# Kernel optimization log

Measured on AMD Instinct MI355X. Metric: run time of the kernel, lower is better.

The kernel has to match this reference:

```python
import jax, jax.numpy as jnp
import numpy as np


def setup_inputs() -> dict:
    key = jax.random.key(0)
    k1, k2 = jax.random.split(key)
    B, S, V = 8, 512, 30522
    logits = jax.random.normal(k1, (B, S, V), dtype=jnp.float32)
    attention_mask = jax.random.randint(k2, (B, S), 0, 2, dtype=jnp.int32)
    return {"logits": logits, "attention_mask": attention_mask, "top_k": 64}


def reference(logits, attention_mask, top_k):
    # Fused SPLADE activation: log1p(relu(logits)) * mask, max-pooled over seq.
    mask = attention_mask.astype(logits.dtype)[:, :, None]        # (B, S, 1)
    activated = jnp.log1p(jax.nn.relu(logits)) * mask             # (B, S, V)
    values = jnp.max(activated, axis=1)                           # (B, V)
    # Top-k thresholding: zero out everything below the k-th largest value.
    top_values, _ = jax.lax.top_k(values, top_k)                  # (B, k)
    threshold = top_values[..., -1, None]                         # (B, 1)
    return values * (values >= threshold).astype(values.dtype)
```

## Files before the change

kernel.cpp:

```cpp
#include <hip/hip_runtime.h>
#include <hip/hip_bf16.h>

constexpr int B_  = 8;
constexpr int S_  = 512;
constexpr int V_  = 30522;
constexpr int V2_ = V_ / 2;
constexpr int V4_ = V_ / 4;

typedef float f32x4 __attribute__((ext_vector_type(4)));

constexpr int K1_THREADS = 1024;
constexpr int VSPLIT  = 4;
constexpr int SLICE4  = 1908;
constexpr int NSCHUNK = 8;
constexpr int SCHUNK  = S_ / NSCHUNK;
constexpr int NSLOT   = 2;

__global__ __launch_bounds__(K1_THREADS)
void splade_max_atomic(const float* __restrict__ logits,
                       const int* __restrict__ mask,
                       unsigned int* __restrict__ out_bits)
{
    __shared__ int s_idx[SCHUNK];
    __shared__ int s_cnt;
    const int vs = blockIdx.x;
    const int sc = blockIdx.y;
    const int b  = blockIdx.z;
    const int s0 = sc * SCHUNK;

    if (threadIdx.x < 64) {
        const int lane = threadIdx.x;
        const int m = mask[b * S_ + s0 + lane] != 0;
        const unsigned long long bal = __ballot(m);
        if (m) s_idx[(int)__popcll(bal & ((1ull << lane) - 1ull))] = lane;
        if (lane == 0) s_cnt = (int)__popcll(bal);
    }
    __syncthreads();
    const int n = s_cnt;

    const int len4 = (vs == VSPLIT - 1) ? (V4_ - vs * SLICE4) : SLICE4;
    int  col4[NSLOT];
    bool valid[NSLOT];
#pragma unroll
    for (int p = 0; p < NSLOT; ++p) {
        const int idx4 = threadIdx.x + p * K1_THREADS;
        valid[p] = (idx4 < len4);
        col4[p]  = valid[p] ? (vs * SLICE4 + idx4) : 0;
    }

    f32x4 acc[NSLOT];
#pragma unroll
    for (int p = 0; p < NSLOT; ++p) acc[p] = (f32x4)(0.f);

    const bool do_tail = (vs == VSPLIT - 1) && (threadIdx.x == 0);
    float tail0 = 0.f, tail1 = 0.f;

    int r = 0;
    for (; r + 1 < n; r += 2) {
        const int s0i = s_idx[r], s1i = s_idx[r + 1];
        const float* r0 = logits + (size_t)(b * S_ + s0 + s0i) * V_;
        const float* r1 = logits + (size_t)(b * S_ + s0 + s1i) * V_;
        f32x4 x0[NSLOT], x1[NSLOT];
#pragma unroll
        for (int p = 0; p < NSLOT; ++p)
            x0[p] = *reinterpret_cast<const f32x4*>(r0 + 4 * col4[p]);
#pragma unroll
        for (int p = 0; p < NSLOT; ++p)
            x1[p] = *reinterpret_cast<const f32x4*>(r1 + 4 * col4[p]);
        if (do_tail) {
            const float2 t0 = *reinterpret_cast<const float2*>(r0 + 2 * (V2_ - 1));
            const float2 t1 = *reinterpret_cast<const float2*>(r1 + 2 * (V2_ - 1));
            tail0 = fmaxf(tail0, fmaxf(t0.x, t1.x));
            tail1 = fmaxf(tail1, fmaxf(t0.y, t1.y));
        }
#pragma unroll
        for (int p = 0; p < NSLOT; ++p) {
#pragma unroll
            for (int q = 0; q < 4; ++q)
                acc[p][q] = fmaxf(acc[p][q], fmaxf(x0[p][q], x1[p][q]));
        }
    }
    if (r < n) {
        const float* r0 = logits + (size_t)(b * S_ + s0 + s_idx[r]) * V_;
        f32x4 x0[NSLOT];
#pragma unroll
        for (int p = 0; p < NSLOT; ++p)
            x0[p] = *reinterpret_cast<const f32x4*>(r0 + 4 * col4[p]);
        if (do_tail) {
            const float2 t0 = *reinterpret_cast<const float2*>(r0 + 2 * (V2_ - 1));
            tail0 = fmaxf(tail0, t0.x);
            tail1 = fmaxf(tail1, t0.y);
        }
#pragma unroll
        for (int p = 0; p < NSLOT; ++p) {
#pragma unroll
            for (int q = 0; q < 4; ++q)
                acc[p][q] = fmaxf(acc[p][q], x0[p][q]);
        }
    }

    unsigned int* o = out_bits + (size_t)b * V_;
#pragma unroll
    for (int p = 0; p < NSLOT; ++p) {
        if (valid[p]) {
#pragma unroll
            for (int q = 0; q < 4; ++q)
                atomicMax(o + 4 * col4[p] + q, __float_as_uint(acc[p][q]));
        }
    }
    if (do_tail) {
        atomicMax(o + 2 * (V2_ - 1),     __float_as_uint(tail0));
        atomicMax(o + 2 * (V2_ - 1) + 1, __float_as_uint(tail1));
    }
}

constexpr int K2_BLOCK = 1024;
constexpr int NPT2 = (V2_ + K2_BLOCK - 1) / K2_BLOCK;

__global__ __launch_bounds__(K2_BLOCK)
void splade_topk_kernel(unsigned int* __restrict__ out_bits,
                        const int* __restrict__ topk_ptr)
{
    const int b = blockIdx.x;
    const int k = topk_ptr[0];
    uint2* row2 = reinterpret_cast<uint2*>(out_bits) + (size_t)b * V2_;

    unsigned int v[2 * NPT2];
#pragma unroll
    for (int i = 0; i < NPT2; ++i) {
        const int idx2 = threadIdx.x + i * K2_BLOCK;
        uint2 x = make_uint2(0u, 0u);
        if (idx2 < V2_) x = row2[idx2];
        v[2 * i]     = x.x;
        v[2 * i + 1] = x.y;
    }

    __shared__ int s_cnt[32];
    for (int i = threadIdx.x; i < 32; i += K2_BLOCK) s_cnt[i] = 0;
    __syncthreads();

    unsigned int lo = 0u, hi = 0x7f800000u;
    for (int it = 0; it < 32; ++it) {
        if (hi - lo <= 1u) break;
        const unsigned int mid = lo + ((hi - lo) >> 1);
        int c = 0;
#pragma unroll
        for (int i = 0; i < 2 * NPT2; ++i)
            c += (int)__popcll(__ballot(v[i] >= mid));
        if ((threadIdx.x & 63) == 0) atomicAdd(&s_cnt[it], c);
        __syncthreads();
        const int cnt = s_cnt[it];
        if (cnt >= k) lo = mid; else hi = mid;
    }

    const unsigned int T = lo;
    float2* frow2 = reinterpret_cast<float2*>(row2);
#pragma unroll
    for (int i = 0; i < NPT2; ++i) {
        const int idx2 = threadIdx.x + i * K2_BLOCK;
        if (idx2 < V2_) {
            const unsigned int a = v[2 * i], c = v[2 * i + 1];
            float rx = 0.0f, ry = 0.0f;
            if (a >= T) rx = log1pf(__uint_as_float(a));
            if (c >= T) ry = log1pf(__uint_as_float(c));
            frow2[idx2] = make_float2(rx, ry);
        }
    }
}

extern "C" void kernel_launch(void* const* d_in, const int* in_sizes, int n_in,
                              void* d_out, int out_size, void* d_ws, size_t ws_size,
                              hipStream_t stream) {
    const float* logits = (const float*)d_in[0];
    const int*   mask   = (const int*)d_in[1];
    const int*   topk   = (const int*)d_in[2];
    unsigned int* out   = (unsigned int*)d_out;

    hipMemsetAsync(out, 0, (size_t)out_size * sizeof(float), stream);

    dim3 g1(VSPLIT, NSCHUNK, B_);
    splade_max_atomic<<<g1, K1_THREADS, 0, stream>>>(logits, mask, out);
    splade_topk_kernel<<<B_, K2_BLOCK, 0, stream>>>(out, topk);
}
```

Baseline: 93.01 us.

## Replace atomicMax reduction with per-chunk partial buffers plus a merge kernel

The seq-max kernel now writes per-sequence-chunk partial maxima into workspace with vector stores instead of issuing scalar atomicMax into the output, and doubles the number of sequence chunks for more blocks. A new merge kernel reduces the 16 partials per (batch, vocab) element, which also removes the memset. This trades atomic traffic for an extra kernel launch and roughly 16x B x V of partial writes and reads.

```diff
diff --git a/kernel.cpp b/kernel.cpp
--- a/kernel.cpp
+++ b/kernel.cpp
@@ -12,14 +12,14 @@
 constexpr int K1_THREADS = 1024;
 constexpr int VSPLIT  = 4;
 constexpr int SLICE4  = 1908;
-constexpr int NSCHUNK = 8;
+constexpr int NSCHUNK = 16;
 constexpr int SCHUNK  = S_ / NSCHUNK;
 constexpr int NSLOT   = 2;
 
 __global__ __launch_bounds__(K1_THREADS)
-void splade_max_atomic(const float* __restrict__ logits,
-                       const int* __restrict__ mask,
-                       unsigned int* __restrict__ out_bits)
+void splade_partial_max(const float* __restrict__ logits,
+                        const int* __restrict__ mask,
+                        float* __restrict__ partial)
 {
     __shared__ int s_idx[SCHUNK];
     __shared__ int s_cnt;
@@ -30,7 +30,7 @@
 
     if (threadIdx.x < 64) {
         const int lane = threadIdx.x;
-        const int m = mask[b * S_ + s0 + lane] != 0;
+        const int m = (lane < SCHUNK) ? (mask[b * S_ + s0 + lane] != 0) : 0;
         const unsigned long long bal = __ballot(m);
         if (m) s_idx[(int)__popcll(bal & ((1ull << lane) - 1ull))] = lane;
         if (lane == 0) s_cnt = (int)__popcll(bal);
@@ -99,40 +99,56 @@
         }
     }
 
-    unsigned int* o = out_bits + (size_t)b * V_;
-#pragma unroll
-    for (int p = 0; p < NSLOT; ++p) {
-        if (valid[p]) {
-#pragma unroll
-            for (int q = 0; q < 4; ++q)
-                atomicMax(o + 4 * col4[p] + q, __float_as_uint(acc[p][q]));
-        }
-    }
+    float* dst = partial + ((size_t)sc * B_ + b) * V_;
+#pragma unroll
+    for (int p = 0; p < NSLOT; ++p)
+        if (valid[p])
+            *reinterpret_cast<f32x4*>(dst + 4 * col4[p]) = acc[p];
     if (do_tail) {
-        atomicMax(o + 2 * (V2_ - 1),     __float_as_uint(tail0));
-        atomicMax(o + 2 * (V2_ - 1) + 1, __float_as_uint(tail1));
-    }
+        dst[2 * (V2_ - 1)]     = tail0;
+        dst[2 * (V2_ - 1) + 1] = tail1;
+    }
+}
+
+constexpr int KM_THREADS  = 256;
+constexpr int KM_BLOCKS_X = (V2_ + KM_THREADS - 1) / KM_THREADS;
+
+__global__ __launch_bounds__(KM_THREADS)
+void splade_merge(const float* __restrict__ partial, float* __restrict__ out)
+{
+    const int b    = blockIdx.y;
+    const int idx2 = blockIdx.x * KM_THREADS + threadIdx.x;
+    if (idx2 >= V2_) return;
+    const float2* p0 = reinterpret_cast<const float2*>(partial) + (size_t)b * V2_ + idx2;
+    float2 m = make_float2(0.0f, 0.0f);
+#pragma unroll
+    for (int gg = 0; gg < NSCHUNK; ++gg) {
+        const float2 x = p0[(size_t)gg * B_ * V2_];
+        m.x = fmaxf(m.x, x.x);
+        m.y = fmaxf(m.y, x.y);
+    }
+    reinterpret_cast<float2*>(out)[(size_t)b * V2_ + idx2] = m;
 }
 
 constexpr int K2_BLOCK = 1024;
 constexpr int NPT2 = (V2_ + K2_BLOCK - 1) / K2_BLOCK;
 
 __global__ __launch_bounds__(K2_BLOCK)
-void splade_topk_kernel(unsigned int* __restrict__ out_bits,
+void splade_topk_kernel(float* __restrict__ out,
                         const int* __restrict__ topk_ptr)
 {
     const int b = blockIdx.x;
     const int k = topk_ptr[0];
-    uint2* row2 = reinterpret_cast<uint2*>(out_bits) + (size_t)b * V2_;
+    float2* row2 = reinterpret_cast<float2*>(out) + (size_t)b * V2_;
 
     unsigned int v[2 * NPT2];
 #pragma unroll
     for (int i = 0; i < NPT2; ++i) {
         const int idx2 = threadIdx.x + i * K2_BLOCK;
-        uint2 x = make_uint2(0u, 0u);
+        float2 x = make_float2(0.0f, 0.0f);
         if (idx2 < V2_) x = row2[idx2];
-        v[2 * i]     = x.x;
-        v[2 * i + 1] = x.y;
+        v[2 * i]     = __float_as_uint(x.x);
+        v[2 * i + 1] = __float_as_uint(x.y);
     }
 
     __shared__ int s_cnt[32];
@@ -154,7 +170,6 @@
     }
 
     const unsigned int T = lo;
-    float2* frow2 = reinterpret_cast<float2*>(row2);
 #pragma unroll
     for (int i = 0; i < NPT2; ++i) {
         const int idx2 = threadIdx.x + i * K2_BLOCK;
@@ -163,7 +178,7 @@
             float rx = 0.0f, ry = 0.0f;
             if (a >= T) rx = log1pf(__uint_as_float(a));
             if (c >= T) ry = log1pf(__uint_as_float(c));
-            frow2[idx2] = make_float2(rx, ry);
+            row2[idx2] = make_float2(rx, ry);
         }
     }
 }
@@ -174,11 +189,12 @@
     const float* logits = (const float*)d_in[0];
     const int*   mask   = (const int*)d_in[1];
     const int*   topk   = (const int*)d_in[2];
-    unsigned int* out   = (unsigned int*)d_out;
-
-    hipMemsetAsync(out, 0, (size_t)out_size * sizeof(float), stream);
+    float*       out    = (float*)d_out;
+    float*       ws     = (float*)d_ws;
 
     dim3 g1(VSPLIT, NSCHUNK, B_);
-    splade_max_atomic<<<g1, K1_THREADS, 0, stream>>>(logits, mask, out);
+    splade_partial_max<<<g1, K1_THREADS, 0, stream>>>(logits, mask, ws);
+    dim3 gm(KM_BLOCKS_X, B_);
+    splade_merge<<<gm, KM_THREADS, 0, stream>>>(ws, out);
     splade_topk_kernel<<<B_, K2_BLOCK, 0, stream>>>(out, topk);
 }
```

After: 81.72 us, median of 2. 1.14x faster.
